# Kernel tuning notes

Measured on AMD Instinct MI355X. Metric: run time of the kernel, lower is better.

The kernel has to match this reference:

```python
import jax, jax.numpy as jnp
import numpy as np

N, SP, SI, K = 256, 64, 32, 8
CIN, C, HEADS, DH = 32, 128, 8, 16
G = 32
OCC_THRESH = 0.7

def _lrelu(x):
    return jax.nn.leaky_relu(x, 0.01)

def _ln(x):
    mu = x.mean(-1, keepdims=True)
    var = ((x - mu) ** 2).mean(-1, keepdims=True)
    return (x - mu) * jax.lax.rsqrt(var + 1e-5)

def _interp3d(vol, coords):
    # vol [C,D,H,W]; coords [...,3] in (z,y,x) voxel-index units -> [..., C]
    v = jnp.moveaxis(vol, 0, -1)
    Dv, Hv, Wv = v.shape[0], v.shape[1], v.shape[2]
    z = jnp.clip(coords[..., 0], 0.0, Dv - 1.0)
    y = jnp.clip(coords[..., 1], 0.0, Hv - 1.0)
    x = jnp.clip(coords[..., 2], 0.0, Wv - 1.0)
    z0 = jnp.floor(z).astype(jnp.int32); y0 = jnp.floor(y).astype(jnp.int32); x0 = jnp.floor(x).astype(jnp.int32)
    z1 = jnp.minimum(z0 + 1, Dv - 1); y1 = jnp.minimum(y0 + 1, Hv - 1); x1 = jnp.minimum(x0 + 1, Wv - 1)
    wz = (z - z0)[..., None]; wy = (y - y0)[..., None]; wx = (x - x0)[..., None]
    c00 = v[z0, y0, x0] * (1 - wx) + v[z0, y0, x1] * wx
    c01 = v[z0, y1, x0] * (1 - wx) + v[z0, y1, x1] * wx
    c10 = v[z1, y0, x0] * (1 - wx) + v[z1, y0, x1] * wx
    c11 = v[z1, y1, x0] * (1 - wx) + v[z1, y1, x1] * wx
    return (c00 * (1 - wy) + c01 * wy) * (1 - wz) + (c10 * (1 - wy) + c11 * wy) * wz

def _tpoints(T, p):
    return p @ T[:3, :3].T + T[:3, 3]

def _rot(T, v):
    return v @ T[:3, :3].T

def _ray_box(o, d, obj_from_cam, dim):
    oo = _tpoints(obj_from_cam, o); dd = _rot(obj_from_cam, d)
    half = dim / 2
    invd = 1.0 / jnp.where(jnp.abs(dd) < 1e-9, 1e-9, dd)
    t0 = (-half - oo) * invd; t1 = (half - oo) * invd
    tlo = jnp.minimum(t0, t1).max(-1); thi = jnp.maximum(t0, t1).min(-1)
    valid = thi >= jnp.maximum(tlo, 0.0)
    return jnp.where(valid, tlo, jnp.inf)

def _attn_block(x, Wqkv, bqkv, Wo, bo, Wf1, bf1, Wf2, bf2):
    # pre-LN MHA over axis -2, then pre-LN FFN; residuals
    h = _ln(x)
    qkv = h @ Wqkv + bqkv
    q, k, v = jnp.split(qkv, 3, axis=-1)
    hd = lambda a: a.reshape(a.shape[:-1] + (HEADS, DH))
    q, k, v = hd(q), hd(k), hd(v)
    s = jnp.einsum('...qhd,...khd->...hqk', q, k) / jnp.sqrt(jnp.float32(DH))
    a = jax.nn.softmax(s, axis=-1)
    o = jnp.einsum('...hqk,...khd->...qhd', a, v)
    o = o.reshape(o.shape[:-2] + (HEADS * DH,)) @ Wo + bo
    x = x + o
    h = _ln(x)
    return x + (_lrelu(h @ Wf1 + bf1) @ Wf2 + bf2)

def setup_inputs() -> dict:
    key = jax.random.key(0)
    ks = jax.random.split(key, 40)
    d = jnp.concatenate([0.25 * (jax.random.uniform(ks[0], (N, 2)) * 2 - 1), jnp.ones((N, 1))], -1)
    rays_d = d / jnp.linalg.norm(d, axis=-1, keepdims=True)
    rays_o = jnp.zeros((N, 3))
    pose = jnp.eye(4).at[2, 3].set(2.0)
    dimension = jnp.ones((3,))
    w = lambda k_, sh: 0.05 * jax.random.normal(k_, sh)
    return {
        'rays_o': rays_o, 'rays_d': rays_d, 'pose': pose, 'dimension': dimension,
        'voxel_probs': jax.random.uniform(ks[1], (G, G, G)),
        'feature_vol': 0.5 * jax.random.normal(ks[2], (CIN, G, G, G)),
        'feature_vol_highres': 0.5 * jax.random.normal(ks[3], (K, 6, G, G, G)),
        'u_primary': jax.random.uniform(ks[4], (N, SP)),
        'u_cat': jax.random.uniform(ks[5], (N, SI)),
        'u_lam': jax.random.uniform(ks[6], (N, SI)),
        'dW1': w(ks[7], (CIN + 1, C)), 'db1': jnp.zeros((C,)),
        'dW2': w(ks[8], (C, 1)), 'db2': jnp.zeros((1,)),
        'rW0': w(ks[9], (CIN + 10, C)), 'rb0': jnp.zeros((C,)),
        'nf_qkv': w(ks[10], (C, 3 * C)), 'nf_qkvb': jnp.zeros((3 * C,)),
        'nf_o': w(ks[11], (C, C)), 'nf_ob': jnp.zeros((C,)),
        'nf_f1': w(ks[12], (C, 2 * C)), 'nf_f1b': jnp.zeros((2 * C,)),
        'nf_f2': w(ks[13], (2 * C, C)), 'nf_f2b': jnp.zeros((C,)),
        'rt_qkv': w(ks[14], (C, 3 * C)), 'rt_qkvb': jnp.zeros((3 * C,)),
        'rt_o': w(ks[15], (C, C)), 'rt_ob': jnp.zeros((C,)),
        'rt_f1': w(ks[16], (C, 2 * C)), 'rt_f1b': jnp.zeros((2 * C,)),
        'rt_f2': w(ks[17], (2 * C, C)), 'rt_f2b': jnp.zeros((C,)),
        'fW': w(ks[18], (C, 3)), 'fb': jnp.zeros((3,)),
        'n_samples_primary': SP, 'n_samples_importance': SI,
    }

def reference(rays_o, rays_d, pose, dimension, voxel_probs, feature_vol, feature_vol_highres,
              u_primary, u_cat, u_lam,
              dW1, db1, dW2, db2, rW0, rb0,
              nf_qkv, nf_qkvb, nf_o, nf_ob, nf_f1, nf_f1b, nf_f2, nf_f2b,
              rt_qkv, rt_qkvb, rt_o, rt_ob, rt_f1, rt_f1b, rt_f2, rt_f2b,
              fW, fb, n_samples_primary, n_samples_importance):
    SPn, SIn = n_samples_primary, n_samples_importance
    ofc = jnp.linalg.inv(pose)  # obj_from_cam
    t_near = _ray_box(rays_o, rays_d, ofc, dimension)
    t_max = t_near + 10.0 * jnp.abs(dimension).sum()
    p_max = rays_o + t_max[:, None] * rays_d
    t_far = t_max - _ray_box(p_max, -rays_d, ofc, dimension)
    m = jnp.isfinite(t_near) & jnp.isfinite(t_far) & (t_far > t_near)
    tn = jnp.where(m, t_near, 0.0); tf = jnp.where(m, t_far, 1.0)
    # stratified primary samples within [t_near, t_far]
    t_coarse = tn[:, None] + (tf - tn)[:, None] * (jnp.arange(SPn, dtype=jnp.float32) + u_primary) / SPn
    get_pts = lambda t: rays_o[:, None] + t[..., None] * rays_d[:, None]
    p_coarse = get_pts(t_coarse)
    def ncoords(p, shp):
        uvz = 0.5 + _tpoints(ofc, p) / dimension
        return uvz[..., ::-1] * (jnp.array(shp, jnp.float32) - 1.0)
    occ_coarse = _interp3d(voxel_probs[None], ncoords(p_coarse, voxel_probs.shape))[..., 0]
    x_coarse = _interp3d(feature_vol, ncoords(p_coarse, feature_vol.shape[-3:]))
    # importance sampling via inverse CDF over adjacent-bin occupancy
    probs = jnp.clip(occ_coarse[:, :-1] + occ_coarse[:, 1:], 1e-12, None)
    cdf = jnp.cumsum(probs, -1)
    cdf = cdf / cdf[:, -1:]
    inds = jnp.clip((u_cat[:, :, None] >= cdf[:, None, :]).sum(-1), 0, SPn - 2)
    t_fine = u_lam * jnp.take_along_axis(t_coarse, inds, -1) + (1 - u_lam) * jnp.take_along_axis(t_coarse, inds + 1, -1)
    p_fine = get_pts(t_fine)
    occ_fine = _interp3d(voxel_probs[None], ncoords(p_fine, voxel_probs.shape))[..., 0]
    x_fine = _interp3d(feature_vol, ncoords(p_fine, feature_vol.shape[-3:]))
    # merge + sort along sample axis
    t_all = jnp.concatenate([t_coarse, t_fine], -1)
    perm = jnp.argsort(t_all, -1)
    t = jnp.take_along_axis(t_all, perm, -1)
    occ = jnp.take_along_axis(jnp.concatenate([occ_coarse, occ_fine], -1), perm, -1)
    p = jnp.take_along_axis(jnp.concatenate([p_coarse, p_fine], -2), perm[..., None], -2)
    x = jnp.take_along_axis(jnp.concatenate([x_coarse, x_fine], -2), perm[..., None], -2)
    # density MLP
    xx = jnp.concatenate([x, occ[..., None]], -1)
    sigma = jax.nn.sigmoid((_lrelu(xx @ dW1 + db1) @ dW2 + db2)[..., 0])
    occ = jnp.where(occ < OCC_THRESH, 0.0, occ)
    alpha = occ * sigma
    # high-res per-view features
    coords_hr = ncoords(p, feature_vol_highres.shape[-3:])
    x_hr = jax.vmap(_interp3d, in_axes=(0, None))(feature_vol_highres, coords_hr)  # [K,N,S,6]
    x_hr = jnp.moveaxis(x_hr, 0, -2)  # [N,S,K,6]
    R = ofc[:3, :3]
    rdo = rays_d @ R.T
    Kv = x_hr.shape[-2]
    bs = x.shape[:2]
    xx2 = jnp.concatenate([
        jnp.broadcast_to(x[:, :, None, :], bs + (Kv, x.shape[-1])),
        x_hr[..., 0:3],
        x_hr[..., 3:6] @ R.T,
        jnp.broadcast_to(rdo[:, None, None, :], bs + (Kv, 3)),
        jnp.broadcast_to(occ[..., None, None], bs + (Kv, 1)),
    ], -1)  # [N,S,K,CIN+10]
    h = xx2 @ rW0 + rb0
    h = _attn_block(h, nf_qkv, nf_qkvb, nf_o, nf_ob, nf_f1, nf_f1b, nf_f2, nf_f2b)  # over views K
    h = h.mean(-2)  # [N,S,C]
    h = _attn_block(h, rt_qkv, rt_qkvb, rt_o, rt_ob, rt_f1, rt_f1b, rt_f2, rt_f2b)  # over samples S
    radiance = jax.nn.sigmoid(h @ fW + fb)  # [N,S,3]
    mk = m[:, None]
    t = jnp.where(mk, t, 0.0)
    occ = jnp.where(mk, occ, 0.0)
    alpha = jnp.where(mk, alpha, 0.0)
    radiance = jnp.where(m[:, None, None], radiance, 0.0)
    # trailing object axis (n_objects=1), matching movedim(0,-1)
    return t[..., None], alpha[..., None], occ[..., None], radiance[..., None]
```

## Files before the change

kernel.cpp:

```cpp
#include <hip/hip_runtime.h>
#include <hip/hip_bf16.h>
#include <cmath>


using bf16 = __hip_bfloat16;
#define DEV __device__ __forceinline__

typedef __attribute__((ext_vector_type(8))) short short8;
typedef __attribute__((ext_vector_type(4))) float f32x4;

DEV float s2f(short s){ unsigned u=((unsigned)(unsigned short)s)<<16; float f; __builtin_memcpy(&f,&u,4); return f; }
DEV short f2s(float f){ bf16 h=__float2bfloat16(f); short r; __builtin_memcpy(&r,&h,2); return r; }

constexpr int NRAY=256, SP=64, SI=32, S=96, KHR=8, CIN=32, C=128, NH=8, DH=16;
constexpr int NT = NRAY*S;
constexpr int MTOT = NT*KHR;

constexpr size_t OFF_RI=0, OFF_TR=9, OFF_M=16, OFF_TN=272, OFF_TF=528, OFF_RDO=784,
  OFF_TS=1552, OFF_OCCS=26128, OFF_OCCT=50704, OFF_CRD=75280, OFF_XS=149008, F32_CNT=935440;

constexpr size_t WT_W0=0, WT_NQKV=8192, WT_NO=57344, WT_NF1=73728, WT_NF2=106496,
  WT_RQKV=139264, WT_RO=188416, WT_RF1=204800, WT_RF2=237568, WT_TOT=270336;
constexpr size_t H2OFF=WT_TOT;
constexpr size_t CHB=H2OFF+(size_t)NT*128;
constexpr size_t RT_TOT=(size_t)NT*512;

struct Corn { int off[8]; float wz, wy, wx; };

DEV void make_corners(float cz, float cy, float cx, Corn& Cn){
  cz=fminf(fmaxf(cz,0.f),31.f); cy=fminf(fmaxf(cy,0.f),31.f); cx=fminf(fmaxf(cx,0.f),31.f);
  int z0=(int)cz, y0=(int)cy, x0=(int)cx;
  int z1=(z0+1<31)?z0+1:31, y1=(y0+1<31)?y0+1:31, x1=(x0+1<31)?x0+1:31;
  Cn.wz=cz-(float)z0; Cn.wy=cy-(float)y0; Cn.wx=cx-(float)x0;
  int zy00=z0*1024+y0*32, zy01=z0*1024+y1*32, zy10=z1*1024+y0*32, zy11=z1*1024+y1*32;
  Cn.off[0]=zy00+x0; Cn.off[1]=zy00+x1;
  Cn.off[2]=zy01+x0; Cn.off[3]=zy01+x1;
  Cn.off[4]=zy10+x0; Cn.off[5]=zy10+x1;
  Cn.off[6]=zy11+x0; Cn.off[7]=zy11+x1;
}

DEV float interp1(const float* __restrict__ vol, const Corn& Cn){
  float v000=vol[Cn.off[0]], v001=vol[Cn.off[1]];
  float v010=vol[Cn.off[2]], v011=vol[Cn.off[3]];
  float v100=vol[Cn.off[4]], v101=vol[Cn.off[5]];
  float v110=vol[Cn.off[6]], v111=vol[Cn.off[7]];
  float wx=Cn.wx, wy=Cn.wy, wz=Cn.wz;
  float c00=v000*(1.f-wx)+v001*wx, c01=v010*(1.f-wx)+v011*wx;
  float c10=v100*(1.f-wx)+v101*wx, c11=v110*(1.f-wx)+v111*wx;
  return (c00*(1.f-wy)+c01*wy)*(1.f-wz) + (c10*(1.f-wy)+c11*wy)*wz;
}

DEV float ray_box(const float* Ri, const float* tr, const float* o3, const float* d3, const float* half){
  float tlo=-INFINITY, thi=INFINITY;
  for(int j=0;j<3;j++){
    float oo=Ri[j*3+0]*o3[0]+Ri[j*3+1]*o3[1]+Ri[j*3+2]*o3[2]+tr[j];
    float dd=Ri[j*3+0]*d3[0]+Ri[j*3+1]*d3[1]+Ri[j*3+2]*d3[2];
    if (fabsf(dd)<1e-9f) dd=1e-9f;
    float inv=1.f/dd;
    float t0=(-half[j]-oo)*inv, t1=(half[j]-oo)*inv;
    tlo=fmaxf(tlo,fminf(t0,t1)); thi=fminf(thi,fmaxf(t0,t1));
  }
  bool valid = thi >= fmaxf(tlo,0.f);
  return valid ? tlo : INFINITY;
}

__global__ __launch_bounds__(64) void k0_setup(
  const float* __restrict__ rays_o, const float* __restrict__ rays_d,
  const float* __restrict__ pose, const float* __restrict__ dimv,
  float* __restrict__ wsf)
{
  __shared__ float Ri[9], tr[3];
  int tid=threadIdx.x; int ray=blockIdx.x*64+tid;
  if(tid==0){
    float P[16];
    for(int j=0;j<16;j++) P[j]=pose[j];
    float a00=P[0],a01=P[1],a02=P[2],a10=P[4],a11=P[5],a12=P[6],a20=P[8],a21=P[9],a22=P[10];
    float c00=a11*a22-a12*a21, c01=a12*a20-a10*a22, c02=a10*a21-a11*a20;
    float det=a00*c00+a01*c01+a02*c02;
    float id=1.f/det;
    Ri[0]=c00*id; Ri[1]=(a02*a21-a01*a22)*id; Ri[2]=(a01*a12-a02*a11)*id;
    Ri[3]=c01*id; Ri[4]=(a00*a22-a02*a20)*id; Ri[5]=(a02*a10-a00*a12)*id;
    Ri[6]=c02*id; Ri[7]=(a01*a20-a00*a21)*id; Ri[8]=(a00*a11-a01*a10)*id;
    float t0=P[3],t1=P[7],t2=P[11];
    tr[0]=-(Ri[0]*t0+Ri[1]*t1+Ri[2]*t2);
    tr[1]=-(Ri[3]*t0+Ri[4]*t1+Ri[5]*t2);
    tr[2]=-(Ri[6]*t0+Ri[7]*t1+Ri[8]*t2);
    if(blockIdx.x==0){
      for(int j=0;j<9;j++) wsf[OFF_RI+j]=Ri[j];
      for(int j=0;j<3;j++) wsf[OFF_TR+j]=tr[j];
    }
  }
  __syncthreads();
  float o3[3],d3[3],dim[3],half[3];
  for(int j=0;j<3;j++){ o3[j]=rays_o[ray*3+j]; d3[j]=rays_d[ray*3+j];
                        dim[j]=dimv[j]; half[j]=0.5f*dim[j]; }
  float tnear=ray_box(Ri,tr,o3,d3,half);
  float tmax=tnear+10.f*(fabsf(dim[0])+fabsf(dim[1])+fabsf(dim[2]));
  float pm[3]={o3[0]+tmax*d3[0], o3[1]+tmax*d3[1], o3[2]+tmax*d3[2]};
  float nd[3]={-d3[0],-d3[1],-d3[2]};
  float tfar=tmax-ray_box(Ri,tr,pm,nd,half);
  bool mm = isfinite(tnear)&&isfinite(tfar)&&(tfar>tnear);
  wsf[OFF_M+ray]=mm?1.f:0.f;
  wsf[OFF_TN+ray]=mm?tnear:0.f;
  wsf[OFF_TF+ray]=mm?tfar:1.f;
  for(int j=0;j<3;j++)
    wsf[OFF_RDO+(size_t)ray*3+j]=Ri[j*3+0]*d3[0]+Ri[j*3+1]*d3[1]+Ri[j*3+2]*d3[2];
}

__global__ __launch_bounds__(128) void k1_sample(
  const float* __restrict__ rays_o, const float* __restrict__ rays_d, const float* __restrict__ dimv,
  const float* __restrict__ voxel, const float* __restrict__ fvol,
  const float* __restrict__ u_p, const float* __restrict__ u_cat, const float* __restrict__ u_lam,
  float* __restrict__ wsf)
{
  int i=blockIdx.x, tid=threadIdx.x;
  __shared__ float Ri[9], tr[3], dim[3], o3[3], d3[3];
  __shared__ float t_all[S], occ_all[S], crd_sh[S][3];
  __shared__ int   coff[S][8];
  __shared__ float cww[S][3];
  __shared__ float cdf[SP];
  __shared__ float totv;
  __shared__ int   rnk[S];
  if(tid<9) Ri[tid]=wsf[OFF_RI+tid];
  if(tid<3){ tr[tid]=wsf[OFF_TR+tid]; dim[tid]=dimv[tid];
             o3[tid]=rays_o[i*3+tid]; d3[tid]=rays_d[i*3+tid]; }
  __syncthreads();
  float tn=wsf[OFF_TN+i], tf=wsf[OFF_TF+i];

  auto do_sample=[&](int s, float t){
    float px=o3[0]+t*d3[0], py=o3[1]+t*d3[1], pz=o3[2]+t*d3[2];
    float q0=Ri[0]*px+Ri[1]*py+Ri[2]*pz+tr[0];
    float q1=Ri[3]*px+Ri[4]*py+Ri[5]*pz+tr[1];
    float q2=Ri[6]*px+Ri[7]*py+Ri[8]*pz+tr[2];
    float cz=(0.5f+q2/dim[2])*31.f;
    float cy=(0.5f+q1/dim[1])*31.f;
    float cx=(0.5f+q0/dim[0])*31.f;
    crd_sh[s][0]=cz; crd_sh[s][1]=cy; crd_sh[s][2]=cx;
    Corn Cn; make_corners(cz,cy,cx,Cn);
    for(int q=0;q<8;q++) coff[s][q]=Cn.off[q];
    cww[s][0]=Cn.wz; cww[s][1]=Cn.wy; cww[s][2]=Cn.wx;
    occ_all[s]=interp1(voxel,Cn);
    t_all[s]=t;
  };

  if(tid<SP){
    float u=u_p[i*SP+tid];
    float t=tn+(tf-tn)*((float)tid+u)*(1.f/64.f);
    do_sample(tid,t);
  }
  __syncthreads();
  if(tid==0){
    float c=0;
    for(int j=0;j<SP-1;j++){ float pr=occ_all[j]+occ_all[j+1]; pr=fmaxf(pr,1e-12f); c+=pr; cdf[j]=c; }
    totv=c;
  }
  __syncthreads();
  if(tid<SP-1) cdf[tid]=cdf[tid]/totv;
  __syncthreads();
  if(tid<SI){
    float u=u_cat[i*SI+tid];
    int cnt=0;
    for(int j=0;j<SP-1;j++) cnt += (u>=cdf[j])?1:0;
    int ind=(cnt<SP-2)?cnt:(SP-2);
    float lam=u_lam[i*SI+tid];
    float tfine=lam*t_all[ind]+(1.f-lam)*t_all[ind+1];
    do_sample(SP+tid,tfine);
  }
  __syncthreads();
  if(tid<S){
    float ts=t_all[tid]; int r=0;
    for(int j=0;j<S;j++){ float tj=t_all[j]; r += (tj<ts || (tj==ts && j<tid)) ? 1:0; }
    rnk[tid]=r;
    size_t base=(size_t)i*S+r;
    wsf[OFF_TS+base]=ts;
    wsf[OFF_OCCS+base]=occ_all[tid];
    wsf[OFF_CRD+base*3+0]=crd_sh[tid][0];
    wsf[OFF_CRD+base*3+1]=crd_sh[tid][1];
    wsf[OFF_CRD+base*3+2]=crd_sh[tid][2];
  }
  __syncthreads();
  for(int idx=tid; idx<S*CIN; idx+=128){
    int s=idx>>5, c=idx&31;
    float wz=cww[s][0], wy=cww[s][1], wx=cww[s][2];
    const float* vc=fvol+(size_t)c*32768;
    float v000=vc[coff[s][0]], v001=vc[coff[s][1]];
    float v010=vc[coff[s][2]], v011=vc[coff[s][3]];
    float v100=vc[coff[s][4]], v101=vc[coff[s][5]];
    float v110=vc[coff[s][6]], v111=vc[coff[s][7]];
    float c00=v000*(1.f-wx)+v001*wx, c01=v010*(1.f-wx)+v011*wx;
    float c10=v100*(1.f-wx)+v101*wx, c11=v110*(1.f-wx)+v111*wx;
    float val=(c00*(1.f-wy)+c01*wy)*(1.f-wz)+(c10*(1.f-wy)+c11*wy)*wz;
    wsf[OFF_XS+((size_t)i*S+rnk[s])*CIN+c]=val;
  }
}

__global__ __launch_bounds__(128) void k2_sigma(
  const float* __restrict__ dW1, const float* __restrict__ db1,
  const float* __restrict__ dW2, const float* __restrict__ db2,
  float* __restrict__ wsf, float* __restrict__ out)
{
  int t=blockIdx.x, tid=threadIdx.x, i=t/S;
  __shared__ float xx[33];
  __shared__ float part[2];
  if(tid<32) xx[tid]=wsf[OFF_XS+(size_t)t*32+tid];
  if(tid==32) xx[32]=wsf[OFF_OCCS+t];
  __syncthreads();
  float acc=db1[tid];
  for(int k=0;k<33;k++) acc=fmaf(xx[k], dW1[k*C+tid], acc);
  acc = acc>=0.f?acc:0.01f*acc;
  float g = acc*dW2[tid];
  for(int off=32;off;off>>=1) g+=__shfl_down(g,off,64);
  if((tid&63)==0) part[tid>>6]=g;
  __syncthreads();
  if(tid==0){
    float z=part[0]+part[1]+db2[0];
    float sg=1.f/(1.f+expf(-z));
    float occ=xx[32];
    float occt=occ<0.7f?0.f:occ;
    float alpha=occt*sg;
    float m=wsf[OFF_M+i];
    float ts=wsf[OFF_TS+t];
    out[t]      =m!=0.f?ts:0.f;
    out[NT+t]   =m!=0.f?alpha:0.f;
    out[2*NT+t] =m!=0.f?occt:0.f;
    wsf[OFF_OCCT+t]=occt;
  }
}

__global__ __launch_bounds__(256) void k_wprep(
  const float* __restrict__ w0, const float* __restrict__ nqkv, const float* __restrict__ no_,
  const float* __restrict__ nf1, const float* __restrict__ nf2,
  const float* __restrict__ rqkv, const float* __restrict__ ro_,
  const float* __restrict__ rf1, const float* __restrict__ rf2,
  short* __restrict__ WT)
{
  int gid = blockIdx.x*256+threadIdx.x;
  if(gid>=(int)WT_TOT) return;
  const float* src; int K,N,Kp; int base;
  if(gid<8192){src=w0;K=42;N=128;Kp=64;base=0;}
  else if(gid<57344){src=nqkv;K=128;N=384;Kp=128;base=8192;}
  else if(gid<73728){src=no_;K=128;N=128;Kp=128;base=57344;}
  else if(gid<106496){src=nf1;K=128;N=256;Kp=128;base=73728;}
  else if(gid<139264){src=nf2;K=256;N=128;Kp=256;base=106496;}
  else if(gid<188416){src=rqkv;K=128;N=384;Kp=128;base=139264;}
  else if(gid<204800){src=ro_;K=128;N=128;Kp=128;base=188416;}
  else if(gid<237568){src=rf1;K=128;N=256;Kp=128;base=204800;}
  else {src=rf2;K=256;N=128;Kp=256;base=237568;}
  int local=gid-base; int n=local/Kp, k=local%Kp;
  WT[gid] = (k<K)? f2s(src[(size_t)k*N+n]) : (short)0;
}

__global__ __launch_bounds__(256) void k_build(
  const float* __restrict__ fvhr, const float* __restrict__ wsf,
  short* __restrict__ X2, int tok0)
{
  int tid=threadIdx.x; int sub=tid>>6, stid=tid&63;
  int tloc=blockIdx.x*4+sub;
  int t=tok0+tloc, i=t/S;
  __shared__ float hr[4][KHR][6];
  __shared__ float xf[4][32];
  __shared__ float RiS[9];
  __shared__ float geo[4][4];
  __shared__ float crd[4][3];
  if(tid<9) RiS[tid]=wsf[OFF_RI+tid];
  if(stid>=16&&stid<19) crd[sub][stid-16]=wsf[OFF_CRD+(size_t)t*3+(stid-16)];
  if(stid>=32) xf[sub][stid-32]=wsf[OFF_XS+(size_t)t*32+(stid-32)];
  if(stid==9) geo[sub][0]=wsf[OFF_OCCT+t];
  if(stid>=12&&stid<15) geo[sub][1+(stid-12)]=wsf[OFF_RDO+(size_t)i*3+(stid-12)];
  __syncthreads();
  if(stid<48){
    int k=stid/6, ch=stid%6;
    Corn Cn; make_corners(crd[sub][0],crd[sub][1],crd[sub][2],Cn);
    hr[sub][k][ch]=interp1(fvhr+(size_t)(k*6+ch)*32768, Cn);
  }
  __syncthreads();
  for(int idx=stid; idx<512; idx+=64){
    int k=idx>>6, j=idx&63; float v;
    if(j<32) v=xf[sub][j];
    else if(j<35) v=hr[sub][k][j-32];
    else if(j<38){int r=j-35; v=hr[sub][k][3]*RiS[r*3+0]+hr[sub][k][4]*RiS[r*3+1]+hr[sub][k][5]*RiS[r*3+2];}
    else if(j<41) v=geo[sub][1+(j-38)];
    else if(j==41) v=geo[sub][0];
    else v=0.f;
    X2[(size_t)(tloc*8+k)*64 + j]=f2s(v);
  }
}

template<int K, bool LNA, bool ACT, bool RESID>
__global__ __launch_bounds__(256) void gemm_ln(
  const short* __restrict__ A, const short* __restrict__ Bt,
  const float* __restrict__ bias, const short* __restrict__ Rres,
  short* __restrict__ Cg, int N)
{
  static_assert(!LNA || K==128, "LNA requires K==128");
  constexpr int KSA = (K<128)?K:128;
  constexpr int NSA = K/KSA;
  constexpr int LDA = KSA+8;
  constexpr int LDB = 64+8;
  __shared__ short Al[128*LDA];
  __shared__ short Bl[128*LDB];
  const int tid=threadIdx.x;
  const int bm=blockIdx.x*128, bn=blockIdx.y*128;
  const int lane=tid&63, wave=tid>>6;
  const int wm=(wave>>1)*64, wn=(wave&1)*64;
  const int quad=lane>>4, m16=lane&15;
  f32x4 acc[4][4];
  for(int a=0;a<4;a++) for(int b=0;b<4;b++) acc[a][b]=(f32x4){0.f,0.f,0.f,0.f};

  for(int sa=0; sa<NSA; ++sa){
    if(sa>0) __syncthreads();
    constexpr int CH8=KSA/8;
    for(int it=0; it<(128*CH8)/256; ++it){
      int li=it*256+tid; int row=li/CH8, kc=li%CH8;
      short8 v = *(const short8*)(A + (size_t)(bm+row)*K + sa*KSA + kc*8);
      if constexpr(LNA){
        float f[8]; float ls=0.f,lq=0.f;
        for(int e=0;e<8;e++){ f[e]=s2f(v[e]); ls+=f[e]; lq+=f[e]*f[e]; }
        for(int off=8;off;off>>=1){ ls+=__shfl_xor(ls,off,16); lq+=__shfl_xor(lq,off,16); }
        float mu=ls*(1.f/128.f);
        float var=lq*(1.f/128.f)-mu*mu;
        float rs=rsqrtf(var+1e-5f);
        for(int e=0;e<8;e++) v[e]=f2s((f[e]-mu)*rs);
      }
      *(short8*)&Al[row*LDA+kc*8]=v;
    }
    __syncthreads();
    for(int sb=0; sb<KSA/64; ++sb){
      if(sb>0) __syncthreads();
      for(int it=0; it<4; ++it){
        int li=it*256+tid; int row=li>>3, kc=li&7;
        *(short8*)&Bl[row*LDB+kc*8] =
          *(const short8*)(Bt + (size_t)(bn+row)*K + sa*KSA + sb*64 + kc*8);
      }
      __syncthreads();
      for(int kk=0; kk<64; kk+=32){
        int ka = sb*64+kk;
        short8 af[4], bfv[4];
        for(int im=0; im<4; im++)
          af[im] = *(const short8*)&Al[(wm+im*16+m16)*LDA + ka + quad*8];
        for(int in=0; in<4; in++)
          bfv[in] = *(const short8*)&Bl[(wn+in*16+m16)*LDB + kk + quad*8];
        for(int im=0;im<4;im++)
          for(int in=0;in<4;in++)
            acc[im][in] = __builtin_amdgcn_mfma_f32_16x16x32_bf16(af[im], bfv[in], acc[im][in], 0,0,0);
      }
    }
  }
  for(int in=0;in<4;in++){
    int col = bn + wn + in*16 + m16;
    float bv = bias[col];
    for(int im=0;im<4;im++){
      for(int r=0;r<4;r++){
        int grow = bm + wm + im*16 + quad*4 + r;
        float v = acc[im][in][r] + bv;
        if constexpr(ACT) v = v>=0.f? v : 0.01f*v;
        if constexpr(RESID) v += s2f(Rres[(size_t)grow*N + col]);
        Cg[(size_t)grow*N + col] = f2s(v);
      }
    }
  }
}

__global__ __launch_bounds__(256) void nf_qkv_attn_o(
  const short* __restrict__ A, const short* __restrict__ Btq,
  const float* __restrict__ bq, const short* __restrict__ Bto,
  const float* __restrict__ bo, short* __restrict__ X1)
{
  __shared__ short Al[32*136];
  __shared__ short U[15360];
  short* Bl = U;
  short* Qt = U;
  const int tid=threadIdx.x;
  const int bm=blockIdx.x*32;
  for(int it=0; it<2; ++it){
    int li=it*256+tid; int row=li>>4, kc=li&15;
    short8 v = *(const short8*)(A + (size_t)(bm+row)*128 + kc*8);
    float f[8]; float ls=0.f,lq=0.f;
    for(int e=0;e<8;e++){ f[e]=s2f(v[e]); ls+=f[e]; lq+=f[e]*f[e]; }
    for(int off=8;off;off>>=1){ ls+=__shfl_xor(ls,off,16); lq+=__shfl_xor(lq,off,16); }
    float mu=ls*(1.f/128.f);
    float var=lq*(1.f/128.f)-mu*mu;
    float rs=rsqrtf(var+1e-5f);
    for(int e=0;e<8;e++) v[e]=f2s((f[e]-mu)*rs);
    *(short8*)&Al[row*136+kc*8]=v;
  }
  const int lane=tid&63, wave=tid>>6;
  const int quad=lane>>4, m16=lane&15;
  const int wn=wave*96;
  f32x4 acc[2][6];
  for(int a=0;a<2;a++) for(int b=0;b<6;b++) acc[a][b]=(f32x4){0.f,0.f,0.f,0.f};
  for(int kc2=0;kc2<4;++kc2){
    __syncthreads();
    for(int it=0; it<6; ++it){
      int li=it*256+tid; int row=li>>2, c=li&3;
      *(short8*)&Bl[row*40+c*8] = *(const short8*)(Btq + (size_t)row*128 + kc2*32 + c*8);
    }
    __syncthreads();
    int ka=kc2*32;
    short8 af[2], bfv[6];
    af[0]=*(const short8*)&Al[m16*136 + ka + quad*8];
    af[1]=*(const short8*)&Al[(16+m16)*136 + ka + quad*8];
    for(int in=0;in<6;in++) bfv[in]=*(const short8*)&Bl[(wn+in*16+m16)*40 + quad*8];
    for(int im=0;im<2;im++)
      for(int in=0;in<6;in++)
        acc[im][in]=__builtin_amdgcn_mfma_f32_16x16x32_bf16(af[im],bfv[in],acc[im][in],0,0,0);
  }
  __syncthreads();
  for(int in=0;in<6;in++){
    int col=wn+in*16+m16;
    float bv=bq[col];
    for(int im=0;im<2;im++)
      for(int r=0;r<4;r++)
        Qt[(im*16+quad*4+r)*392+col]=f2s(acc[im][in][r]+bv);
  }
  __syncthreads();
  int tok=tid>>6, h=(tid>>3)&7, q=tid&7;
  const short* base=&Qt[(tok*8)*392 + h*16];
  short8 q0v=*(const short8*)&base[q*392];
  short8 q1v=*(const short8*)&base[q*392+8];
  float qv[16];
  for(int e=0;e<8;e++){ qv[e]=s2f(q0v[e]); qv[8+e]=s2f(q1v[e]); }
  float sc[8]; float mx=-INFINITY;
  for(int j=0;j<8;j++){
    short8 k0=*(const short8*)&base[j*392+128];
    short8 k1=*(const short8*)&base[j*392+136];
    float a=0;
    for(int e=0;e<8;e++) a += qv[e]*s2f(k0[e]) + qv[8+e]*s2f(k1[e]);
    a*=0.25f; sc[j]=a; mx=fmaxf(mx,a);
  }
  float se=0;
  for(int j=0;j<8;j++){ sc[j]=expf(sc[j]-mx); se+=sc[j]; }
  float inv=1.f/se;
  float o[16];
  for(int d=0;d<16;d++) o[d]=0.f;
  for(int j=0;j<8;j++){
    short8 v0=*(const short8*)&base[j*392+256];
    short8 v1=*(const short8*)&base[j*392+264];
    float p=sc[j];
    for(int e=0;e<8;e++){ o[e]=fmaf(p,s2f(v0[e]),o[e]); o[8+e]=fmaf(p,s2f(v1[e]),o[8+e]); }
  }
  short8 o0,o1;
  for(int e=0;e<8;e++){ o0[e]=f2s(o[e]*inv); o1[e]=f2s(o[8+e]*inv); }
  __syncthreads();
  {
    int r = tok*8+q;
    *(short8*)&U[r*136 + h*16]     = o0;
    *(short8*)&U[r*136 + h*16 + 8] = o1;
  }
  short* Wl = U + 4352;
  const int wn2 = wave*32;
  f32x4 acc2[2][2];
  for(int a=0;a<2;a++) for(int b=0;b<2;b++) acc2[a][b]=(f32x4){0.f,0.f,0.f,0.f};
  for(int kc2=0;kc2<4;++kc2){
    __syncthreads();
    for(int it=0; it<2; ++it){
      int li=it*256+tid; int row=li>>2, c=li&3;
      *(short8*)&Wl[row*40+c*8] = *(const short8*)(Bto + (size_t)row*128 + kc2*32 + c*8);
    }
    __syncthreads();
    int ka=kc2*32;
    short8 af[2], bfv[2];
    af[0]=*(const short8*)&U[m16*136 + ka + quad*8];
    af[1]=*(const short8*)&U[(16+m16)*136 + ka + quad*8];
    for(int in=0;in<2;in++) bfv[in]=*(const short8*)&Wl[(wn2+in*16+m16)*40 + quad*8];
    for(int im=0;im<2;im++)
      for(int in=0;in<2;in++)
        acc2[im][in]=__builtin_amdgcn_mfma_f32_16x16x32_bf16(af[im],bfv[in],acc2[im][in],0,0,0);
  }
  for(int in=0;in<2;in++){
    int col=wn2+in*16+m16;
    float bv=bo[col];
    for(int im=0;im<2;im++)
      for(int r=0;r<4;r++){
        int grow=bm+im*16+quad*4+r;
        float v=acc2[im][in][r]+bv + s2f(A[(size_t)grow*128+col]);
        X1[(size_t)grow*128+col]=f2s(v);
      }
  }
}

__global__ __launch_bounds__(256) void nf_f1f2(
  const short* __restrict__ X1, const short* __restrict__ Bt1, const float* __restrict__ b1,
  const short* __restrict__ Bt2, const float* __restrict__ b2,
  short* __restrict__ H2)
{
  __shared__ short LB[8448 + 10240];
  short* Al = LB;
  short* F1 = LB;
  short* Bl = LB + 8448;
  const int tid=threadIdx.x;
  const int bm=blockIdx.x*32;
  for(int it=0; it<2; ++it){
    int li=it*256+tid; int row=li>>4, kc=li&15;
    short8 v = *(const short8*)(X1 + (size_t)(bm+row)*128 + kc*8);
    float f[8]; float ls=0.f,lq=0.f;
    for(int e=0;e<8;e++){ f[e]=s2f(v[e]); ls+=f[e]; lq+=f[e]*f[e]; }
    for(int off=8;off;off>>=1){ ls+=__shfl_xor(ls,off,16); lq+=__shfl_xor(lq,off,16); }
    float mu=ls*(1.f/128.f);
    float var=lq*(1.f/128.f)-mu*mu;
    float rs=rsqrtf(var+1e-5f);
    for(int e=0;e<8;e++) v[e]=f2s((f[e]-mu)*rs);
    *(short8*)&Al[row*136+kc*8]=v;
  }
  const int lane=tid&63, wave=tid>>6;
  const int quad=lane>>4, m16=lane&15;
  {
    const int wn=wave*64;
    f32x4 acc[2][4];
    for(int a=0;a<2;a++) for(int b=0;b<4;b++) acc[a][b]=(f32x4){0.f,0.f,0.f,0.f};
    for(int kc2=0;kc2<4;++kc2){
      __syncthreads();
      for(int it=0; it<4; ++it){
        int li=it*256+tid; int row=li>>2, c=li&3;
        *(short8*)&Bl[row*40+c*8] = *(const short8*)(Bt1 + (size_t)row*128 + kc2*32 + c*8);
      }
      __syncthreads();
      int ka=kc2*32;
      short8 af[2], bfv[4];
      af[0]=*(const short8*)&Al[m16*136 + ka + quad*8];
      af[1]=*(const short8*)&Al[(16+m16)*136 + ka + quad*8];
      for(int in=0;in<4;in++) bfv[in]=*(const short8*)&Bl[(wn+in*16+m16)*40 + quad*8];
      for(int im=0;im<2;im++)
        for(int in=0;in<4;in++)
          acc[im][in]=__builtin_amdgcn_mfma_f32_16x16x32_bf16(af[im],bfv[in],acc[im][in],0,0,0);
    }
    __syncthreads();
    for(int in=0;in<4;in++){
      int col=wn+in*16+m16;
      float bv=b1[col];
      for(int im=0;im<2;im++)
        for(int r=0;r<4;r++){
          float v=acc[im][in][r]+bv;
          v = v>=0.f? v : 0.01f*v;
          F1[(im*16+quad*4+r)*264+col]=f2s(v);
        }
    }
  }
  __syncthreads();
  {
    const int wn=wave*32;
    f32x4 acc[2][2];
    for(int a=0;a<2;a++) for(int b=0;b<2;b++) acc[a][b]=(f32x4){0.f,0.f,0.f,0.f};
    for(int kc2=0;kc2<8;++kc2){
      __syncthreads();
      for(int it=0; it<2; ++it){
        int li=it*256+tid; int row=li>>2, c=li&3;
        *(short8*)&Bl[row*40+c*8] = *(const short8*)(Bt2 + (size_t)row*256 + kc2*32 + c*8);
      }
      __syncthreads();
      int ka=kc2*32;
      short8 af[2], bfv[2];
      af[0]=*(const short8*)&F1[m16*264 + ka + quad*8];
      af[1]=*(const short8*)&F1[(16+m16)*264 + ka + quad*8];
      for(int in=0;in<2;in++) bfv[in]=*(const short8*)&Bl[(wn+in*16+m16)*40 + quad*8];
      for(int im=0;im<2;im++)
        for(int in=0;in<2;in++)
          acc[im][in]=__builtin_amdgcn_mfma_f32_16x16x32_bf16(af[im],bfv[in],acc[im][in],0,0,0);
    }
    for(int in=0;in<2;in++){
      int col=wn+in*16+m16;
      float bv=b2[col];
      for(int im=0;im<2;im++){
        float s4=0.f;
        for(int r=0;r<4;r++){
          int grow=bm+im*16+quad*4+r;
          float v=acc[im][in][r]+bv + s2f(X1[(size_t)grow*128+col]);
          s4+=v;
        }
        float stok = s4 + __shfl_xor(s4,16,64);
        if((quad&1)==0){
          int tok=((bm+im*16)>>3)+(quad>>1);
          H2[(size_t)tok*128+col]=f2s(stok*0.125f);
        }
      }
    }
  }
}

__global__ __launch_bounds__(256) void rt_attn(const short* __restrict__ qkvb, short* __restrict__ attout){
  int b=blockIdx.x; int i=b&255, h0=(b>>8)*4; int tid=threadIdx.x;
  __shared__ float kh[96][64], vh[96][64];
  for(int idx=tid; idx<1536; idx+=256){
    int kv = idx>=768; int l = idx - kv*768;
    int j = l>>3, c = l&7;
    size_t base = ((size_t)(i*96+j))*384 + h0*16 + (kv?256:128) + c*8;
    short8 x = *(const short8*)(qkvb+base);
    float* dst = kv? &vh[j][c*8] : &kh[j][c*8];
    for(int e=0;e<8;e++) dst[e]=s2f(x[e]);
  }
  __syncthreads();
  int jh=tid>>7, t2=tid&127;
  int hh=t2>>5, lq=t2&31, h=h0+hh, r0=lq*3;
  float q[3][16];
  for(int rr=0;rr<3;rr++){
    size_t qb=((size_t)(i*96+r0+rr))*384 + h*16;
    short8 a=*(const short8*)(qkvb+qb), bq=*(const short8*)(qkvb+qb+8);
    for(int e=0;e<8;e++){ q[rr][e]=s2f(a[e]); q[rr][8+e]=s2f(bq[e]); }
  }
  float acc[3][16]; float se[3]={0.f,0.f,0.f};
  for(int rr=0;rr<3;rr++) for(int d=0;d<16;d++) acc[rr][d]=0.f;
  const float* kb=&kh[jh*48][hh*16];
  const float* vb=&vh[jh*48][hh*16];
  for(int j=0;j<48;j++){
    const float* kj = kb + j*64;
    float s0=0.f,s1=0.f,s2=0.f;
    for(int d=0;d<16;d++){ float kv_=kj[d];
      s0=fmaf(q[0][d],kv_,s0); s1=fmaf(q[1][d],kv_,s1); s2=fmaf(q[2][d],kv_,s2); }
    float p0=expf(s0*0.25f), p1=expf(s1*0.25f), p2=expf(s2*0.25f);
    se[0]+=p0; se[1]+=p1; se[2]+=p2;
    const float* vj = vb + j*64;
    for(int d=0;d<16;d++){ float vv=vj[d];
      acc[0][d]=fmaf(p0,vv,acc[0][d]); acc[1][d]=fmaf(p1,vv,acc[1][d]); acc[2][d]=fmaf(p2,vv,acc[2][d]); }
  }
  __syncthreads();
  float* pacc=(float*)kh;
  float* pse =(float*)vh;
  if(jh==1){
    for(int rr=0;rr<3;rr++){
      for(int d=0;d<16;d++) pacc[(t2*3+rr)*16+d]=acc[rr][d];
      pse[t2*3+rr]=se[rr];
    }
  }
  __syncthreads();
  if(jh==0){
    for(int rr=0;rr<3;rr++){
      float sv = se[rr] + pse[t2*3+rr];
      float inv = 1.f/sv;
      short8 o0,o1;
      for(int e=0;e<8;e++){
        float a0=acc[rr][e]   + pacc[(t2*3+rr)*16+e];
        float a1=acc[rr][8+e] + pacc[(t2*3+rr)*16+8+e];
        o0[e]=f2s(a0*inv); o1[e]=f2s(a1*inv);
      }
      size_t ob=((size_t)(i*96+r0+rr))*128 + h*16;
      *(short8*)(attout+ob)=o0;
      *(short8*)(attout+ob+8)=o1;
    }
  }
}

__global__ __launch_bounds__(256) void k_rad(
  const short* __restrict__ h3, const float* __restrict__ fW, const float* __restrict__ fb,
  const float* __restrict__ wsf, float* __restrict__ out)
{
  int t=blockIdx.x*256+threadIdx.x;
  if(t>=NT) return;
  int i=t/S;
  float a0=fb[0], a1=fb[1], a2=fb[2];
  for(int c=0;c<C;c++){
    float hv=s2f(h3[(size_t)t*C+c]);
    a0=fmaf(hv,fW[c*3+0],a0);
    a1=fmaf(hv,fW[c*3+1],a1);
    a2=fmaf(hv,fW[c*3+2],a2);
  }
  float m=wsf[OFF_M+i];
  float r0=1.f/(1.f+expf(-a0)), r1=1.f/(1.f+expf(-a1)), r2=1.f/(1.f+expf(-a2));
  size_t ob=3*(size_t)NT+(size_t)t*3;
  out[ob+0]=m!=0.f?r0:0.f;
  out[ob+1]=m!=0.f?r1:0.f;
  out[ob+2]=m!=0.f?r2:0.f;
}

extern "C" void kernel_launch(void* const* d_in, const int* in_sizes, int n_in,
                              void* d_out, int out_size, void* d_ws, size_t ws_size,
                              hipStream_t stream) {
  (void)in_sizes; (void)n_in; (void)out_size;
  const float* rays_o =(const float*)d_in[0];
  const float* rays_d =(const float*)d_in[1];
  const float* pose   =(const float*)d_in[2];
  const float* dimv   =(const float*)d_in[3];
  const float* voxel  =(const float*)d_in[4];
  const float* fvol   =(const float*)d_in[5];
  const float* fvhr   =(const float*)d_in[6];
  const float* u_p    =(const float*)d_in[7];
  const float* u_cat  =(const float*)d_in[8];
  const float* u_lam  =(const float*)d_in[9];
  const float* dW1    =(const float*)d_in[10];
  const float* db1    =(const float*)d_in[11];
  const float* dW2    =(const float*)d_in[12];
  const float* db2    =(const float*)d_in[13];
  const float* rW0    =(const float*)d_in[14];
  const float* rb0    =(const float*)d_in[15];
  const float* nf_qkv =(const float*)d_in[16];
  const float* nf_qkvb=(const float*)d_in[17];
  const float* nf_o   =(const float*)d_in[18];
  const float* nf_ob  =(const float*)d_in[19];
  const float* nf_f1  =(const float*)d_in[20];
  const float* nf_f1b =(const float*)d_in[21];
  const float* nf_f2  =(const float*)d_in[22];
  const float* nf_f2b =(const float*)d_in[23];
  const float* rt_qkv =(const float*)d_in[24];
  const float* rt_qkvb=(const float*)d_in[25];
  const float* rt_o   =(const float*)d_in[26];
  const float* rt_ob  =(const float*)d_in[27];
  const float* rt_f1  =(const float*)d_in[28];
  const float* rt_f1b =(const float*)d_in[29];
  const float* rt_f2  =(const float*)d_in[30];
  const float* rt_f2b =(const float*)d_in[31];
  const float* fW     =(const float*)d_in[32];
  const float* fb     =(const float*)d_in[33];

  float* wsf=(float*)d_ws;
  short* wsb=(short*)((char*)d_ws + F32_CNT*4);
  float* out=(float*)d_out;

  int nch=8;
  for(int c=1;c<=8;c<<=1){
    size_t mc_=(size_t)MTOT/c;
    size_t region=mc_*640ULL; if(region<RT_TOT) region=RT_TOT;
    size_t need=F32_CNT*4 + 2ULL*(CHB + region);
    if(need <= ws_size){ nch=c; break; }
  }
  const size_t mc = (size_t)MTOT/nch;
  const int Tc = (int)(mc/8);

  short* WT  = wsb;
  short* H2  = wsb + H2OFF;
  short* arena = wsb + CHB;
  short* o_h0 = arena;
  short* o_x1 = arena + (size_t)128*mc;
  short* o_x2 = arena + (size_t)512*mc;
  short* r_qkv= arena;
  short* r_att= arena + (size_t)384*NT;
  short* r_x  = arena;
  short* r_f1 = arena + (size_t)128*NT;
  short* r_h3 = arena + (size_t)384*NT;

  k0_setup<<<NRAY/64,64,0,stream>>>(rays_o,rays_d,pose,dimv,wsf);
  k1_sample<<<NRAY,128,0,stream>>>(rays_o,rays_d,dimv,voxel,fvol,u_p,u_cat,u_lam,wsf);
  k2_sigma<<<NT,128,0,stream>>>(dW1,db1,dW2,db2,wsf,out);
  k_wprep<<<(int)((WT_TOT+255)/256),256,0,stream>>>(rW0,nf_qkv,nf_o,nf_f1,nf_f2,rt_qkv,rt_o,rt_f1,rt_f2,WT);

  const int mt=(int)(mc/128);
  const int mt32=(int)(mc/32);
  for(int ch=0; ch<nch; ++ch){
    int tok0 = ch*Tc;
    k_build<<<Tc/4,256,0,stream>>>(fvhr, wsf, o_x2, tok0);
    gemm_ln< 64,false,false,false><<<dim3(mt,1),256,0,stream>>>(o_x2, WT+WT_W0,  rb0,     nullptr, o_h0, 128);
    nf_qkv_attn_o<<<mt32,256,0,stream>>>(o_h0, WT+WT_NQKV, nf_qkvb, WT+WT_NO, nf_ob, o_x1);
    nf_f1f2<<<mt32,256,0,stream>>>(o_x1, WT+WT_NF1, nf_f1b, WT+WT_NF2, nf_f2b,
                                   H2+(size_t)tok0*128);
  }

  gemm_ln<128,true ,false,false><<<dim3(NT/128,3),256,0,stream>>>(H2,   WT+WT_RQKV,rt_qkvb, nullptr, r_qkv,384);
  rt_attn<<<NRAY*2,256,0,stream>>>(r_qkv, r_att);
  gemm_ln<128,false,false,true ><<<dim3(NT/128,1),256,0,stream>>>(r_att,WT+WT_RO,  rt_ob,   H2,      r_x,  128);
  gemm_ln<128,true ,true ,false><<<dim3(NT/128,2),256,0,stream>>>(r_x,  WT+WT_RF1, rt_f1b,  nullptr, r_f1, 256);
  gemm_ln<256,false,false,true ><<<dim3(NT/128,1),256,0,stream>>>(r_f1, WT+WT_RF2, rt_f2b,  r_x,     r_h3, 128);
  k_rad<<<NT/256,256,0,stream>>>(r_h3, fW, fb, wsf, out);
}
```

Baseline: 466.4 us.

## Fuse per-view input projection, attention, and FFN into a single block kernel

Merges the W0 input GEMM, the QKV/attention/output-projection kernel, and the FFN kernel into one kernel per 32-row tile. Intermediates h0 and x1 stay in LDS and registers instead of going through global memory, and residuals come from registers. This removes two launches per chunk and the global round trips of the [M,128] activations. In exchange, LDS use per block rises (about 48KB), which may lower occupancy.

```diff
diff --git a/kernel.cpp b/kernel.cpp
--- a/kernel.cpp
+++ b/kernel.cpp
@@ -361,49 +361,85 @@
   }
 }
 
-__global__ __launch_bounds__(256) void nf_qkv_attn_o(
-  const short* __restrict__ A, const short* __restrict__ Btq,
-  const float* __restrict__ bq, const short* __restrict__ Bto,
-  const float* __restrict__ bo, short* __restrict__ X1)
+__global__ __launch_bounds__(256) void nf_block(
+  const short* __restrict__ X2,
+  const short* __restrict__ Bw0, const float* __restrict__ b0,
+  const short* __restrict__ Btq, const float* __restrict__ bq,
+  const short* __restrict__ Bto, const float* __restrict__ bo,
+  const short* __restrict__ Bt1, const float* __restrict__ b1,
+  const short* __restrict__ Bt2, const float* __restrict__ b2,
+  short* __restrict__ H2)
 {
-  __shared__ short Al[32*136];
   __shared__ short U[15360];
-  short* Bl = U;
-  short* Qt = U;
+  __shared__ short hL[4352];
+  __shared__ short xL[4352];
   const int tid=threadIdx.x;
   const int bm=blockIdx.x*32;
+  const int lane=tid&63, wave=tid>>6;
+  const int quad=lane>>4, m16=lane&15;
+  const int wns=wave*32;
+
+  {
+    int row=tid>>3, kc=tid&7;
+    *(short8*)&U[row*72+kc*8] = *(const short8*)(X2 + (size_t)(bm+row)*64 + kc*8);
+  }
+  short* Bw = U + 2304;
+  f32x4 accA[2][2];
+  for(int a=0;a<2;a++) for(int b=0;b<2;b++) accA[a][b]=(f32x4){0.f,0.f,0.f,0.f};
+  for(int kc2=0;kc2<2;++kc2){
+    __syncthreads();
+    for(int it=0; it<2; ++it){
+      int li=it*256+tid; int row=li>>2, c=li&3;
+      *(short8*)&Bw[row*40+c*8] = *(const short8*)(Bw0 + (size_t)row*64 + kc2*32 + c*8);
+    }
+    __syncthreads();
+    int ka=kc2*32;
+    short8 af[2], bfv[2];
+    af[0]=*(const short8*)&U[m16*72 + ka + quad*8];
+    af[1]=*(const short8*)&U[(16+m16)*72 + ka + quad*8];
+    for(int in=0;in<2;in++) bfv[in]=*(const short8*)&Bw[(wns+in*16+m16)*40 + quad*8];
+    for(int im=0;im<2;im++) for(int in=0;in<2;in++)
+      accA[im][in]=__builtin_amdgcn_mfma_f32_16x16x32_bf16(af[im],bfv[in],accA[im][in],0,0,0);
+  }
+  float h0r[2][2][4];
+  for(int in=0;in<2;in++){
+    int col=wns+in*16+m16;
+    float bv=b0[col];
+    for(int im=0;im<2;im++)
+      for(int r=0;r<4;r++){
+        short hv=f2s(accA[im][in][r]+bv);
+        h0r[im][in][r]=s2f(hv);
+        hL[(im*16+quad*4+r)*136+col]=hv;
+      }
+  }
+  __syncthreads();
   for(int it=0; it<2; ++it){
     int li=it*256+tid; int row=li>>4, kc=li&15;
-    short8 v = *(const short8*)(A + (size_t)(bm+row)*128 + kc*8);
+    short8 v=*(short8*)&hL[row*136+kc*8];
     float f[8]; float ls=0.f,lq=0.f;
     for(int e=0;e<8;e++){ f[e]=s2f(v[e]); ls+=f[e]; lq+=f[e]*f[e]; }
     for(int off=8;off;off>>=1){ ls+=__shfl_xor(ls,off,16); lq+=__shfl_xor(lq,off,16); }
-    float mu=ls*(1.f/128.f);
-    float var=lq*(1.f/128.f)-mu*mu;
-    float rs=rsqrtf(var+1e-5f);
+    float mu=ls*(1.f/128.f), var=lq*(1.f/128.f)-mu*mu, rs=rsqrtf(var+1e-5f);
     for(int e=0;e<8;e++) v[e]=f2s((f[e]-mu)*rs);
-    *(short8*)&Al[row*136+kc*8]=v;
-  }
-  const int lane=tid&63, wave=tid>>6;
-  const int quad=lane>>4, m16=lane&15;
+    *(short8*)&hL[row*136+kc*8]=v;
+  }
   const int wn=wave*96;
-  f32x4 acc[2][6];
-  for(int a=0;a<2;a++) for(int b=0;b<6;b++) acc[a][b]=(f32x4){0.f,0.f,0.f,0.f};
+  f32x4 acc6[2][6];
+  for(int a=0;a<2;a++) for(int b=0;b<6;b++) acc6[a][b]=(f32x4){0.f,0.f,0.f,0.f};
   for(int kc2=0;kc2<4;++kc2){
     __syncthreads();
     for(int it=0; it<6; ++it){
       int li=it*256+tid; int row=li>>2, c=li&3;
-      *(short8*)&Bl[row*40+c*8] = *(const short8*)(Btq + (size_t)row*128 + kc2*32 + c*8);
+      *(short8*)&U[row*40+c*8] = *(const short8*)(Btq + (size_t)row*128 + kc2*32 + c*8);
     }
     __syncthreads();
     int ka=kc2*32;
     short8 af[2], bfv[6];
-    af[0]=*(const short8*)&Al[m16*136 + ka + quad*8];
-    af[1]=*(const short8*)&Al[(16+m16)*136 + ka + quad*8];
-    for(int in=0;in<6;in++) bfv[in]=*(const short8*)&Bl[(wn+in*16+m16)*40 + quad*8];
-    for(int im=0;im<2;im++)
-      for(int in=0;in<6;in++)
-        acc[im][in]=__builtin_amdgcn_mfma_f32_16x16x32_bf16(af[im],bfv[in],acc[im][in],0,0,0);
+    af[0]=*(const short8*)&hL[m16*136 + ka + quad*8];
+    af[1]=*(const short8*)&hL[(16+m16)*136 + ka + quad*8];
+    for(int in=0;in<6;in++) bfv[in]=*(const short8*)&U[(wn+in*16+m16)*40 + quad*8];
+    for(int im=0;im<2;im++) for(int in=0;in<6;in++)
+      acc6[im][in]=__builtin_amdgcn_mfma_f32_16x16x32_bf16(af[im],bfv[in],acc6[im][in],0,0,0);
   }
   __syncthreads();
   for(int in=0;in<6;in++){
@@ -411,11 +447,11 @@
     float bv=bq[col];
     for(int im=0;im<2;im++)
       for(int r=0;r<4;r++)
-        Qt[(im*16+quad*4+r)*392+col]=f2s(acc[im][in][r]+bv);
+        U[(im*16+quad*4+r)*392+col]=f2s(acc6[im][in][r]+bv);
   }
   __syncthreads();
   int tok=tid>>6, h=(tid>>3)&7, q=tid&7;
-  const short* base=&Qt[(tok*8)*392 + h*16];
+  const short* base=&U[(tok*8)*392 + h*16];
   short8 q0v=*(const short8*)&base[q*392];
   short8 q1v=*(const short8*)&base[q*392+8];
   float qv[16];
@@ -443,135 +479,106 @@
   for(int e=0;e<8;e++){ o0[e]=f2s(o[e]*inv); o1[e]=f2s(o[8+e]*inv); }
   __syncthreads();
   {
-    int r = tok*8+q;
-    *(short8*)&U[r*136 + h*16]     = o0;
-    *(short8*)&U[r*136 + h*16 + 8] = o1;
-  }
-  short* Wl = U + 4352;
-  const int wn2 = wave*32;
-  f32x4 acc2[2][2];
-  for(int a=0;a<2;a++) for(int b=0;b<2;b++) acc2[a][b]=(f32x4){0.f,0.f,0.f,0.f};
+    int r=tok*8+q;
+    *(short8*)&hL[r*136+h*16]  =o0;
+    *(short8*)&hL[r*136+h*16+8]=o1;
+  }
+  for(int a=0;a<2;a++) for(int b=0;b<2;b++) accA[a][b]=(f32x4){0.f,0.f,0.f,0.f};
   for(int kc2=0;kc2<4;++kc2){
     __syncthreads();
     for(int it=0; it<2; ++it){
       int li=it*256+tid; int row=li>>2, c=li&3;
-      *(short8*)&Wl[row*40+c*8] = *(const short8*)(Bto + (size_t)row*128 + kc2*32 + c*8);
+      *(short8*)&U[row*40+c*8] = *(const short8*)(Bto + (size_t)row*128 + kc2*32 + c*8);
     }
     __syncthreads();
     int ka=kc2*32;
     short8 af[2], bfv[2];
-    af[0]=*(const short8*)&U[m16*136 + ka + quad*8];
-    af[1]=*(const short8*)&U[(16+m16)*136 + ka + quad*8];
-    for(int in=0;in<2;in++) bfv[in]=*(const short8*)&Wl[(wn2+in*16+m16)*40 + quad*8];
-    for(int im=0;im<2;im++)
-      for(int in=0;in<2;in++)
-        acc2[im][in]=__builtin_amdgcn_mfma_f32_16x16x32_bf16(af[im],bfv[in],acc2[im][in],0,0,0);
-  }
+    af[0]=*(const short8*)&hL[m16*136 + ka + quad*8];
+    af[1]=*(const short8*)&hL[(16+m16)*136 + ka + quad*8];
+    for(int in=0;in<2;in++) bfv[in]=*(const short8*)&U[(wns+in*16+m16)*40 + quad*8];
+    for(int im=0;im<2;im++) for(int in=0;in<2;in++)
+      accA[im][in]=__builtin_amdgcn_mfma_f32_16x16x32_bf16(af[im],bfv[in],accA[im][in],0,0,0);
+  }
+  float x1r[2][2][4];
   for(int in=0;in<2;in++){
-    int col=wn2+in*16+m16;
+    int col=wns+in*16+m16;
     float bv=bo[col];
     for(int im=0;im<2;im++)
       for(int r=0;r<4;r++){
-        int grow=bm+im*16+quad*4+r;
-        float v=acc2[im][in][r]+bv + s2f(A[(size_t)grow*128+col]);
-        X1[(size_t)grow*128+col]=f2s(v);
-      }
-  }
-}
-
-__global__ __launch_bounds__(256) void nf_f1f2(
-  const short* __restrict__ X1, const short* __restrict__ Bt1, const float* __restrict__ b1,
-  const short* __restrict__ Bt2, const float* __restrict__ b2,
-  short* __restrict__ H2)
-{
-  __shared__ short LB[8448 + 10240];
-  short* Al = LB;
-  short* F1 = LB;
-  short* Bl = LB + 8448;
-  const int tid=threadIdx.x;
-  const int bm=blockIdx.x*32;
+        short xv=f2s(accA[im][in][r]+bv+h0r[im][in][r]);
+        x1r[im][in][r]=s2f(xv);
+        xL[(im*16+quad*4+r)*136+col]=xv;
+      }
+  }
+  __syncthreads();
   for(int it=0; it<2; ++it){
     int li=it*256+tid; int row=li>>4, kc=li&15;
-    short8 v = *(const short8*)(X1 + (size_t)(bm+row)*128 + kc*8);
+    short8 v=*(short8*)&xL[row*136+kc*8];
     float f[8]; float ls=0.f,lq=0.f;
     for(int e=0;e<8;e++){ f[e]=s2f(v[e]); ls+=f[e]; lq+=f[e]*f[e]; }
     for(int off=8;off;off>>=1){ ls+=__shfl_xor(ls,off,16); lq+=__shfl_xor(lq,off,16); }
-    float mu=ls*(1.f/128.f);
-    float var=lq*(1.f/128.f)-mu*mu;
-    float rs=rsqrtf(var+1e-5f);
+    float mu=ls*(1.f/128.f), var=lq*(1.f/128.f)-mu*mu, rs=rsqrtf(var+1e-5f);
     for(int e=0;e<8;e++) v[e]=f2s((f[e]-mu)*rs);
-    *(short8*)&Al[row*136+kc*8]=v;
-  }
-  const int lane=tid&63, wave=tid>>6;
-  const int quad=lane>>4, m16=lane&15;
-  {
-    const int wn=wave*64;
-    f32x4 acc[2][4];
-    for(int a=0;a<2;a++) for(int b=0;b<4;b++) acc[a][b]=(f32x4){0.f,0.f,0.f,0.f};
-    for(int kc2=0;kc2<4;++kc2){
-      __syncthreads();
-      for(int it=0; it<4; ++it){
-        int li=it*256+tid; int row=li>>2, c=li&3;
-        *(short8*)&Bl[row*40+c*8] = *(const short8*)(Bt1 + (size_t)row*128 + kc2*32 + c*8);
-      }
-      __syncthreads();
-      int ka=kc2*32;
-      short8 af[2], bfv[4];
-      af[0]=*(const short8*)&Al[m16*136 + ka + quad*8];
-      af[1]=*(const short8*)&Al[(16+m16)*136 + ka + quad*8];
-      for(int in=0;in<4;in++) bfv[in]=*(const short8*)&Bl[(wn+in*16+m16)*40 + quad*8];
-      for(int im=0;im<2;im++)
-        for(int in=0;in<4;in++)
-          acc[im][in]=__builtin_amdgcn_mfma_f32_16x16x32_bf16(af[im],bfv[in],acc[im][in],0,0,0);
-    }
-    __syncthreads();
-    for(int in=0;in<4;in++){
-      int col=wn+in*16+m16;
-      float bv=b1[col];
-      for(int im=0;im<2;im++)
-        for(int r=0;r<4;r++){
-          float v=acc[im][in][r]+bv;
-          v = v>=0.f? v : 0.01f*v;
-          F1[(im*16+quad*4+r)*264+col]=f2s(v);
-        }
-    }
-  }
-  __syncthreads();
-  {
-    const int wn=wave*32;
-    f32x4 acc[2][2];
-    for(int a=0;a<2;a++) for(int b=0;b<2;b++) acc[a][b]=(f32x4){0.f,0.f,0.f,0.f};
-    for(int kc2=0;kc2<8;++kc2){
-      __syncthreads();
-      for(int it=0; it<2; ++it){
-        int li=it*256+tid; int row=li>>2, c=li&3;
-        *(short8*)&Bl[row*40+c*8] = *(const short8*)(Bt2 + (size_t)row*256 + kc2*32 + c*8);
-      }
-      __syncthreads();
-      int ka=kc2*32;
-      short8 af[2], bfv[2];
-      af[0]=*(const short8*)&F1[m16*264 + ka + quad*8];
-      af[1]=*(const short8*)&F1[(16+m16)*264 + ka + quad*8];
-      for(int in=0;in<2;in++) bfv[in]=*(const short8*)&Bl[(wn+in*16+m16)*40 + quad*8];
-      for(int im=0;im<2;im++)
-        for(int in=0;in<2;in++)
-          acc[im][in]=__builtin_amdgcn_mfma_f32_16x16x32_bf16(af[im],bfv[in],acc[im][in],0,0,0);
-    }
-    for(int in=0;in<2;in++){
-      int col=wn+in*16+m16;
-      float bv=b2[col];
-      for(int im=0;im<2;im++){
-        float s4=0.f;
-        for(int r=0;r<4;r++){
-          int grow=bm+im*16+quad*4+r;
-          float v=acc[im][in][r]+bv + s2f(X1[(size_t)grow*128+col]);
-          s4+=v;
-        }
-        float stok = s4 + __shfl_xor(s4,16,64);
-        if((quad&1)==0){
-          int tok=((bm+im*16)>>3)+(quad>>1);
-          H2[(size_t)tok*128+col]=f2s(stok*0.125f);
-        }
+    *(short8*)&xL[row*136+kc*8]=v;
+  }
+  const int wn1=wave*64;
+  f32x4 acc4[2][4];
+  for(int a=0;a<2;a++) for(int b=0;b<4;b++) acc4[a][b]=(f32x4){0.f,0.f,0.f,0.f};
+  for(int kc2=0;kc2<4;++kc2){
+    __syncthreads();
+    for(int it=0; it<4; ++it){
+      int li=it*256+tid; int row=li>>2, c=li&3;
+      *(short8*)&U[row*40+c*8] = *(const short8*)(Bt1 + (size_t)row*128 + kc2*32 + c*8);
+    }
+    __syncthreads();
+    int ka=kc2*32;
+    short8 af[2], bfv[4];
+    af[0]=*(const short8*)&xL[m16*136 + ka + quad*8];
+    af[1]=*(const short8*)&xL[(16+m16)*136 + ka + quad*8];
+    for(int in=0;in<4;in++) bfv[in]=*(const short8*)&U[(wn1+in*16+m16)*40 + quad*8];
+    for(int im=0;im<2;im++) for(int in=0;in<4;in++)
+      acc4[im][in]=__builtin_amdgcn_mfma_f32_16x16x32_bf16(af[im],bfv[in],acc4[im][in],0,0,0);
+  }
+  __syncthreads();
+  for(int in=0;in<4;in++){
+    int col=wn1+in*16+m16;
+    float bv=b1[col];
+    for(int im=0;im<2;im++)
+      for(int r=0;r<4;r++){
+        float v=acc4[im][in][r]+bv;
+        v = v>=0.f? v : 0.01f*v;
+        U[(im*16+quad*4+r)*264+col]=f2s(v);
+      }
+  }
+  __syncthreads();
+  short* B2l = U + 8448;
+  f32x4 accB[2][2];
+  for(int a=0;a<2;a++) for(int b=0;b<2;b++) accB[a][b]=(f32x4){0.f,0.f,0.f,0.f};
+  for(int kc2=0;kc2<8;++kc2){
+    __syncthreads();
+    for(int it=0; it<2; ++it){
+      int li=it*256+tid; int row=li>>2, c=li&3;
+      *(short8*)&B2l[row*40+c*8] = *(const short8*)(Bt2 + (size_t)row*256 + kc2*32 + c*8);
+    }
+    __syncthreads();
+    int ka=kc2*32;
+    short8 af[2], bfv[2];
+    af[0]=*(const short8*)&U[m16*264 + ka + quad*8];
+    af[1]=*(const short8*)&U[(16+m16)*264 + ka + quad*8];
+    for(int in=0;in<2;in++) bfv[in]=*(const short8*)&B2l[(wns+in*16+m16)*40 + quad*8];
+    for(int im=0;im<2;im++) for(int in=0;in<2;in++)
+      accB[im][in]=__builtin_amdgcn_mfma_f32_16x16x32_bf16(af[im],bfv[in],accB[im][in],0,0,0);
+  }
+  for(int in=0;in<2;in++){
+    int col=wns+in*16+m16;
+    float bv=b2[col];
+    for(int im=0;im<2;im++){
+      float s4=0.f;
+      for(int r=0;r<4;r++) s4 += accB[im][in][r]+bv+x1r[im][in][r];
+      float stok = s4 + __shfl_xor(s4,16,64);
+      if((quad&1)==0){
+        int tokk=((bm+im*16)>>3)+(quad>>1);
+        H2[(size_t)tokk*128+col]=f2s(stok*0.125f);
       }
     }
   }
@@ -717,8 +724,6 @@
   short* WT  = wsb;
   short* H2  = wsb + H2OFF;
   short* arena = wsb + CHB;
-  short* o_h0 = arena;
-  short* o_x1 = arena + (size_t)128*mc;
   short* o_x2 = arena + (size_t)512*mc;
   short* r_qkv= arena;
   short* r_att= arena + (size_t)384*NT;
@@ -731,15 +736,14 @@
   k2_sigma<<<NT,128,0,stream>>>(dW1,db1,dW2,db2,wsf,out);
   k_wprep<<<(int)((WT_TOT+255)/256),256,0,stream>>>(rW0,nf_qkv,nf_o,nf_f1,nf_f2,rt_qkv,rt_o,rt_f1,rt_f2,WT);
 
-  const int mt=(int)(mc/128);
   const int mt32=(int)(mc/32);
   for(int ch=0; ch<nch; ++ch){
     int tok0 = ch*Tc;
     k_build<<<Tc/4,256,0,stream>>>(fvhr, wsf, o_x2, tok0);
-    gemm_ln< 64,false,false,false><<<dim3(mt,1),256,0,stream>>>(o_x2, WT+WT_W0,  rb0,     nullptr, o_h0, 128);
-    nf_qkv_attn_o<<<mt32,256,0,stream>>>(o_h0, WT+WT_NQKV, nf_qkvb, WT+WT_NO, nf_ob, o_x1);
-    nf_f1f2<<<mt32,256,0,stream>>>(o_x1, WT+WT_NF1, nf_f1b, WT+WT_NF2, nf_f2b,
-                                   H2+(size_t)tok0*128);
+    nf_block<<<mt32,256,0,stream>>>(o_x2,
+      WT+WT_W0, rb0, WT+WT_NQKV, nf_qkvb, WT+WT_NO, nf_ob,
+      WT+WT_NF1, nf_f1b, WT+WT_NF2, nf_f2b,
+      H2+(size_t)tok0*128);
   }
 
   gemm_ln<128,true ,false,false><<<dim3(NT/128,3),256,0,stream>>>(H2,   WT+WT_RQKV,rt_qkvb, nullptr, r_qkv,384);
```

Result: slower. 491.4 us (+5.4%).
